# Optimization experiments

Measured on AMD Instinct MI355X. Metric: run time of the kernel, lower is better.

## Reference

```python
import jax, jax.numpy as jnp
import numpy as np

NV, NE = 4096, 8192
FV, FE = 128, 64
FV_OUT = 128


def setup_inputs() -> dict:
    key = jax.random.key(0)
    ks = jax.random.split(key, 8)
    stdv = 1.0 / np.sqrt(FV_OUT)
    return {
        "H_v": jax.random.normal(ks[0], (NV, FV), dtype=jnp.float32),
        "H_e": jax.random.normal(ks[1], (NE, FE), dtype=jnp.float32),
        "adj_e": jax.random.uniform(ks[2], (NE, NE), dtype=jnp.float32),
        "adj_v": jax.random.uniform(ks[3], (NV, NV), dtype=jnp.float32),
        "T": jax.random.uniform(ks[4], (NV, NE), dtype=jnp.float32),
        "weight": jax.random.uniform(ks[5], (FV, FV_OUT), minval=-stdv, maxval=stdv, dtype=jnp.float32),
        "p": jax.random.normal(ks[6], (1, FE), dtype=jnp.float32),
        "bias": jax.random.uniform(ks[7], (FV_OUT,), minval=-stdv, maxval=stdv, dtype=jnp.float32),
    }


def reference(H_v, H_e, adj_e, adj_v, T, weight, p, bias):
    # node_layer=True path of GraphConvolution.forward
    # d = (H_e @ p.T) as a vector over edges; T @ diag(d) == T * d[None, :]
    d = (H_e @ p.T)[:, 0]                       # [Ne]
    multiplier = (T * d[None, :]) @ T.T         # [Nv, Nv]
    n = multiplier.shape[0]
    mask = jnp.eye(n, dtype=multiplier.dtype)   # eye mask: diag -> 1, off-diag -> multiplier
    M1 = mask + (1.0 - mask) * multiplier
    adjusted_A = M1 * adj_v                     # elementwise mask with dense adjacency
    output = adjusted_A @ (H_v @ weight) + bias # [Nv, Fv_out]
    return (output, H_e)
```

## Files before the change

kernel.cpp:

```cpp
#include <hip/hip_runtime.h>
#include <stdint.h>

#define NV 4096
#define NE 8192
#define FV 128
#define FE 64
#define FOUT 128

typedef unsigned short u16;
typedef __attribute__((ext_vector_type(8))) short short8;
typedef __attribute__((ext_vector_type(4))) float f32x4;
typedef __attribute__((ext_vector_type(4))) unsigned short u16x4;

__device__ __forceinline__ u16 f2bf(float f) {
  uint32_t u = __builtin_bit_cast(uint32_t, f);
  u += 0x7fffu + ((u >> 16) & 1u);
  return (u16)(u >> 16);
}
__device__ __forceinline__ float bf2f(u16 h) {
  return __builtin_bit_cast(float, (uint32_t)h << 16);
}

#define AS1(p) ((__attribute__((address_space(1))) void*)(void*)(p))
#define AS3(p) ((__attribute__((address_space(3))) void*)(p))

__global__ __launch_bounds__(256) void k_edge_dot(const float* __restrict__ He,
                                                  const float* __restrict__ p,
                                                  float* __restrict__ d,
                                                  float* __restrict__ out) {
  const int lane = threadIdx.x & 63;
  const int gw = blockIdx.x * 4 + (threadIdx.x >> 6);
  const float pv = p[lane];
  for (int e = gw; e < NE; e += 512) {
    float h = He[(size_t)e * FE + lane];
    out[(size_t)NV * FOUT + (size_t)e * FE + lane] = h;
    float v = h * pv;
    #pragma unroll
    for (int off = 32; off > 0; off >>= 1) v += __shfl_down(v, off);
    if (lane == 0) d[e] = v;
  }
}

__global__ __launch_bounds__(256) void k_convert(const float* __restrict__ T,
                                                 const float* __restrict__ d,
                                                 u16* __restrict__ Ta,
                                                 u16* __restrict__ Tb) {
  size_t idx = ((size_t)blockIdx.x * 256 + threadIdx.x) * 8;
  f32x4 t0 = *(const f32x4*)&T[idx];
  f32x4 t1 = *(const f32x4*)&T[idx + 4];
  int e = (int)(idx & (NE - 1));
  f32x4 d0 = *(const f32x4*)&d[e];
  f32x4 d1 = *(const f32x4*)&d[e + 4];
  short8 a, b;
  a[0] = (short)f2bf(t0.x * d0.x); a[1] = (short)f2bf(t0.y * d0.y);
  a[2] = (short)f2bf(t0.z * d0.z); a[3] = (short)f2bf(t0.w * d0.w);
  a[4] = (short)f2bf(t1.x * d1.x); a[5] = (short)f2bf(t1.y * d1.y);
  a[6] = (short)f2bf(t1.z * d1.z); a[7] = (short)f2bf(t1.w * d1.w);
  b[0] = (short)f2bf(t0.x); b[1] = (short)f2bf(t0.y);
  b[2] = (short)f2bf(t0.z); b[3] = (short)f2bf(t0.w);
  b[4] = (short)f2bf(t1.x); b[5] = (short)f2bf(t1.y);
  b[6] = (short)f2bf(t1.z); b[7] = (short)f2bf(t1.w);
  *(short8*)&Ta[idx] = a;
  *(short8*)&Tb[idx] = b;
}

__global__ __launch_bounds__(256) void k_hw(const float* __restrict__ Hv,
                                            const float* __restrict__ W,
                                            u16* __restrict__ HWt) {
  __shared__ float sW[FV * FOUT];
  __shared__ float sH[8 * FV];
  const int tid = threadIdx.x;
  const int i0 = blockIdx.x * 8;
  #pragma unroll
  for (int k = 0; k < 16; ++k)
    *(f32x4*)&sW[k * 1024 + tid * 4] = *(const f32x4*)&W[k * 1024 + tid * 4];
  *(f32x4*)&sH[tid * 4] = *(const f32x4*)&Hv[(size_t)i0 * FV + tid * 4];
  __syncthreads();
  const int n = tid & 127;
  const int rh = tid >> 7;
  float acc[4] = {0.f, 0.f, 0.f, 0.f};
  #pragma unroll 4
  for (int f = 0; f < FV; ++f) {
    float wv = sW[f * FOUT + n];
    #pragma unroll
    for (int rr = 0; rr < 4; ++rr)
      acc[rr] += sH[(rh * 4 + rr) * FV + f] * wv;
  }
  #pragma unroll
  for (int rr = 0; rr < 4; ++rr)
    HWt[(size_t)n * NV + i0 + rh * 4 + rr] = f2bf(acc[rr]);
}

__global__ __launch_bounds__(512, 2) void k_gemm_m(const u16* __restrict__ Ta,
                                                   const u16* __restrict__ Tb,
                                                   const float* __restrict__ adjv,
                                                   u16* __restrict__ adjA) {
  __shared__ __align__(16) u16 smem[66560];

  const int bi = blockIdx.x >> 4;
  const int bj = blockIdx.x & 15;
  const int tile_m = bi * 256;
  const int tile_n = bj * 256;
  const int tid = threadIdx.x;
  const int lane = tid & 63;
  const int wid = tid >> 6;
  const int wr = wid >> 2;
  const int wc = wid & 3;
  const int row16 = lane & 15;
  const int quad = lane >> 4;
  const int swz8 = (quad ^ ((row16 >> 1) & 3)) * 8;

  const int srow = tid >> 2;
  const int sslot = (tid & 3) ^ ((tid >> 3) & 3);
  const u16* gA0 = Ta + (size_t)(tile_m + srow) * NE + sslot * 8;
  const u16* gA1 = gA0 + (size_t)128 * NE;
  const u16* gB0 = Tb + (size_t)(tile_n + srow) * NE + sslot * 8;
  const u16* gB1 = gB0 + (size_t)128 * NE;
  const int ldsO0 = (wid * 64) * 8;
  const int ldsO1 = (512 + wid * 64) * 8;

#define STG(gp0, gp1, roff, kcol)                                                                 \
  do {                                                                                            \
    __builtin_amdgcn_global_load_lds(AS1((gp0) + (kcol)), AS3(&smem[(roff) + ldsO0]), 16, 0, 0);  \
    __builtin_amdgcn_global_load_lds(AS1((gp1) + (kcol)), AS3(&smem[(roff) + ldsO1]), 16, 0, 0);  \
  } while (0)

  f32x4 acc[8][4] = {};
  short8 aX[4], aY[4], bX[4], bY[4];

  const int arow32 = (wr * 128 + row16) * 32 + swz8;
  const int brow32 = (wc * 64 + row16) * 32 + swz8;

#define LDSA(b, kk, mh, DST)                                                                   \
  do { _Pragma("unroll")                                                                       \
    for (int m2 = 0; m2 < 4; ++m2)                                                             \
      DST[m2] = *(const short8*)&smem[(b)*16384 + (kk)*8192 + arow32 + ((mh)*4 + m2) * 512];   \
  } while (0)

#define LDSB(b, kk, DST)                                                                       \
  do { _Pragma("unroll")                                                                       \
    for (int ni = 0; ni < 4; ++ni)                                                             \
      DST[ni] = *(const short8*)&smem[32768 + (b)*16384 + (kk)*8192 + brow32 + ni * 512];      \
  } while (0)

#define MMP(mh, ASET, BSET)                                                                                 \
  do { _Pragma("unroll")                                                                                    \
    for (int m2 = 0; m2 < 4; ++m2) { _Pragma("unroll")                                                      \
      for (int ni = 0; ni < 4; ++ni)                                                                        \
        acc[(mh)*4+m2][ni] = __builtin_amdgcn_mfma_f32_16x16x32_bf16(ASET[m2], BSET[ni], acc[(mh)*4+m2][ni], 0,0,0); \
    }                                                                                                       \
  } while (0)

#define BARF()  do { __builtin_amdgcn_s_barrier(); asm volatile("" ::: "memory"); } while (0)
#define WAITK(k) do { asm volatile("s_waitcnt lgkmcnt(" #k ")" ::: "memory"); \
                      __builtin_amdgcn_sched_barrier(0); } while (0)
#define GATE8() asm volatile("s_waitcnt vmcnt(8)" ::: "memory")
#define PRIO1() __builtin_amdgcn_s_setprio(1)
#define PRIO0() __builtin_amdgcn_s_setprio(0)

  STG(gB0, gB1, 32768, 0);
  STG(gA0, gA1, 0,     0);
  STG(gB0, gB1, 40960, 32);
  STG(gA0, gA1, 8192,  32);
  STG(gB0, gB1, 49152, 64);
  STG(gA0, gA1, 16384, 64);
  STG(gB0, gB1, 57344, 96);
  asm volatile("s_waitcnt vmcnt(10)" ::: "memory");
  BARF();
  LDSB(0, 0, bX);
  LDSA(0, 0, 0, aX);

  #pragma unroll 1
  for (int it = 0; it < 64; ++it) {
    const int t = it * 2;
    const int k1 = (t + 1) * 64;
    const int k2 = (t + 2 < 128 ? t + 2 : 127) * 64;
    const int k3 = (t + 3 < 128 ? t + 3 : 127) * 64;

    LDSA(0, 0, 1, aY);
    STG(gA0, gA1, 24576, k1 + 32);
    WAITK(4);
    PRIO1(); MMP(0, aX, bX); PRIO0();
    GATE8(); BARF();

    LDSB(0, 1, bY); LDSA(0, 1, 0, aX);
    STG(gB0, gB1, 32768, k2);
    WAITK(8);
    PRIO1(); MMP(1, aY, bX); PRIO0();
    BARF();

    LDSA(0, 1, 1, aY);
    STG(gA0, gA1, 0, k2);
    WAITK(4);
    PRIO1(); MMP(0, aX, bY); PRIO0();
    GATE8(); BARF();

    LDSB(1, 0, bX); LDSA(1, 0, 0, aX);
    STG(gB0, gB1, 40960, k2 + 32);
    WAITK(8);
    PRIO1(); MMP(1, aY, bY); PRIO0();
    BARF();

    LDSA(1, 0, 1, aY);
    STG(gA0, gA1, 8192, k2 + 32);
    WAITK(4);
    PRIO1(); MMP(0, aX, bX); PRIO0();
    GATE8(); BARF();

    LDSB(1, 1, bY); LDSA(1, 1, 0, aX);
    STG(gB0, gB1, 49152, k3);
    WAITK(8);
    PRIO1(); MMP(1, aY, bX); PRIO0();
    BARF();

    LDSA(1, 1, 1, aY);
    STG(gA0, gA1, 16384, k3);
    WAITK(4);
    PRIO1(); MMP(0, aX, bY); PRIO0();
    GATE8(); BARF();

    LDSB(0, 0, bX); LDSA(0, 0, 0, aX);
    STG(gB0, gB1, 57344, k3 + 32);
    WAITK(8);
    PRIO1(); MMP(1, aY, bY); PRIO0();
    BARF();
  }

  asm volatile("s_waitcnt vmcnt(0) lgkmcnt(0)" ::: "memory");
  __syncthreads();
  #pragma unroll
  for (int mi = 0; mi < 8; ++mi) {
    #pragma unroll
    for (int ni = 0; ni < 4; ++ni) {
      const int row = wr * 128 + mi * 16 + quad * 4;
      const int col = wc * 64 + ni * 16 + row16;
      #pragma unroll
      for (int r = 0; r < 4; ++r)
        smem[(row + r) * 260 + col] = f2bf(acc[mi][ni][r]);
    }
  }
  __syncthreads();
  const int ep_r = tid >> 4;
  const int ep_c = (tid & 15) * 4;
  for (int pass = 0; pass < 8; ++pass) {
    const int row = pass * 32 + ep_r;
    const int gr = tile_m + row;
    const size_t gbase = (size_t)gr * NV + tile_n;
    #pragma unroll
    for (int j = 0; j < 4; ++j) {
      const int col = ep_c + j * 64;
      const int gc = tile_n + col;
      u16x4 m4 = *(const u16x4*)&smem[row * 260 + col];
      f32x4 av = *(const f32x4*)&adjv[gbase + col];
      u16x4 o;
      o.x = f2bf(((gr == gc + 0) ? 1.0f : bf2f(m4.x)) * av.x);
      o.y = f2bf(((gr == gc + 1) ? 1.0f : bf2f(m4.y)) * av.y);
      o.z = f2bf(((gr == gc + 2) ? 1.0f : bf2f(m4.z)) * av.z);
      o.w = f2bf(((gr == gc + 3) ? 1.0f : bf2f(m4.w)) * av.w);
      *(u16x4*)&adjA[gbase + col] = o;
    }
  }

#undef STG
#undef LDSA
#undef LDSB
#undef MMP
#undef BARF
#undef WAITK
#undef GATE8
#undef PRIO1
#undef PRIO0
}

#define KSPLIT 8
__global__ __launch_bounds__(256) void k_gemm_out(const u16* __restrict__ A,
                                                  const u16* __restrict__ B,
                                                  float* __restrict__ part) {
  __shared__ __align__(16) u16 lA[128 * 32];
  __shared__ __align__(16) u16 lB[128 * 32];
  const int K = NV;
  const int tile_m = blockIdx.y * 128;
  const int kbeg = blockIdx.x * (K / KSPLIT);
  const int kend = kbeg + (K / KSPLIT);
  const int tid = threadIdx.x;
  const int lane = tid & 63;
  const int wave = tid >> 6;
  const int wm = (wave >> 1) * 64;
  const int wn = (wave & 1) * 64;
  const int row16 = lane & 15;
  const int quad = lane >> 4;

  f32x4 acc[4][4] = {};

  for (int k0 = kbeg; k0 < kend; k0 += 32) {
    __syncthreads();
    #pragma unroll
    for (int r = 0; r < 2; ++r) {
      const int chunk = r * 256 + wave * 64 + lane;
      const int row = chunk >> 2;
      const int cc = chunk & 3;
      const u16* ga = A + ((size_t)(tile_m + row) * K + k0 + cc * 8);
      const u16* gb = B + ((size_t)row * K + k0 + cc * 8);
      __builtin_amdgcn_global_load_lds(AS1(ga), AS3(&lA[(r * 256 + wave * 64) * 8]), 16, 0, 0);
      __builtin_amdgcn_global_load_lds(AS1(gb), AS3(&lB[(r * 256 + wave * 64) * 8]), 16, 0, 0);
    }
    __syncthreads();
    short8 a[4], b[4];
    #pragma unroll
    for (int mi = 0; mi < 4; ++mi)
      a[mi] = *(const short8*)&lA[(wm + mi * 16 + row16) * 32 + quad * 8];
    #pragma unroll
    for (int ni = 0; ni < 4; ++ni)
      b[ni] = *(const short8*)&lB[(wn + ni * 16 + row16) * 32 + quad * 8];
    #pragma unroll
    for (int mi = 0; mi < 4; ++mi)
      #pragma unroll
      for (int ni = 0; ni < 4; ++ni)
        acc[mi][ni] = __builtin_amdgcn_mfma_f32_16x16x32_bf16(a[mi], b[ni], acc[mi][ni], 0, 0, 0);
  }

  float* pdst = part + (size_t)blockIdx.x * NV * FOUT;
  #pragma unroll
  for (int mi = 0; mi < 4; ++mi) {
    #pragma unroll
    for (int ni = 0; ni < 4; ++ni) {
      const int gc = wn + ni * 16 + row16;
      #pragma unroll
      for (int r = 0; r < 4; ++r) {
        const int gr = tile_m + wm + mi * 16 + quad * 4 + r;
        pdst[(size_t)gr * FOUT + gc] = acc[mi][ni][r];
      }
    }
  }
}

__global__ __launch_bounds__(256) void k_reduce(const float* __restrict__ part,
                                                const float* __restrict__ bias,
                                                float* __restrict__ out) {
  size_t idx = ((size_t)blockIdx.x * 256 + threadIdx.x) * 4;
  f32x4 s = *(const f32x4*)&bias[idx & (FOUT - 1)];
  #pragma unroll
  for (int ks = 0; ks < KSPLIT; ++ks)
    s += *(const f32x4*)&part[(size_t)ks * NV * FOUT + idx];
  *(f32x4*)&out[idx] = s;
}

extern "C" void kernel_launch(void* const* d_in, const int* in_sizes, int n_in,
                              void* d_out, int out_size, void* d_ws, size_t ws_size,
                              hipStream_t stream) {
  const float* Hv   = (const float*)d_in[0];
  const float* He   = (const float*)d_in[1];
  const float* adjv = (const float*)d_in[3];
  const float* T    = (const float*)d_in[4];
  const float* W    = (const float*)d_in[5];
  const float* p    = (const float*)d_in[6];
  const float* bias = (const float*)d_in[7];
  float* out = (float*)d_out;

  char* ws = (char*)d_ws;
  float* dvec = (float*)ws;
  u16* HWt    = (u16*)(ws + ((size_t)1 << 20));
  u16* Ta     = (u16*)(ws + ((size_t)2 << 20));
  u16* Tb     = (u16*)(ws + ((size_t)2 << 20) + ((size_t)64 << 20));
  u16* adjA   = (u16*)(ws + ((size_t)2 << 20) + ((size_t)128 << 20));
  float* part = (float*)(ws + ((size_t)2 << 20) + ((size_t)160 << 20));

  k_edge_dot<<<128, 256, 0, stream>>>(He, p, dvec, out);
  k_convert<<<(NV * NE) / (256 * 8), 256, 0, stream>>>(T, dvec, Ta, Tb);
  k_hw<<<NV / 8, 256, 0, stream>>>(Hv, W, HWt);
  k_gemm_m<<<256, 512, 0, stream>>>(Ta, Tb, adjv, adjA);
  k_gemm_out<<<dim3(KSPLIT, NV / 128), 256, 0, stream>>>(adjA, HWt, part);
  k_reduce<<<(NV * FOUT) / (256 * 4), 256, 0, stream>>>(part, bias, out);
}
```

Measured before the change: 674.7 us.

## Switch multiplier GEMM to 32x32x16 MFMA with restructured LDS swizzle and waits

Replaces the 16x16x32 bf16 MFMA tiling in the T·diag(d)·T^T GEMM with 32x32x16 MFMA instructions. This changes the per-wave fragment layout, the LDS read swizzle, the staging slot swizzle and the epilogue register-to-row mapping. It also drops register double-buffering of fragments in favour of load-then-wait (lgkmcnt(0)) with an extra barrier per phase, and removes the unroll-1 pragma. The larger MFMA shape cuts LDS reads per FLOP and instruction count. In exchange, the full lgkm waits and extra barriers serialize LDS loads against MFMA work.

```diff
diff --git a/kernel.cpp b/kernel.cpp
--- a/kernel.cpp
+++ b/kernel.cpp
@@ -10,6 +10,7 @@
 typedef unsigned short u16;
 typedef __attribute__((ext_vector_type(8))) short short8;
 typedef __attribute__((ext_vector_type(4))) float f32x4;
+typedef __attribute__((ext_vector_type(16))) float f32x16;
 typedef __attribute__((ext_vector_type(4))) unsigned short u16x4;
 
 __device__ __forceinline__ u16 f2bf(float f) {
@@ -106,12 +107,14 @@
   const int wid = tid >> 6;
   const int wr = wid >> 2;
   const int wc = wid & 3;
-  const int row16 = lane & 15;
-  const int quad = lane >> 4;
-  const int swz8 = (quad ^ ((row16 >> 1) & 3)) * 8;
+  const int row32 = lane & 31;
+  const int hi = lane >> 5;
+
+  const int swz0 = ((hi)     ^ (row32 & 3)) * 8;
+  const int swz1 = ((2 + hi) ^ (row32 & 3)) * 8;
 
   const int srow = tid >> 2;
-  const int sslot = (tid & 3) ^ ((tid >> 3) & 3);
+  const int sslot = (tid & 3) ^ ((tid >> 2) & 3);
   const u16* gA0 = Ta + (size_t)(tile_m + srow) * NE + sslot * 8;
   const u16* gA1 = gA0 + (size_t)128 * NE;
   const u16* gB0 = Tb + (size_t)(tile_n + srow) * NE + sslot * 8;
@@ -125,36 +128,45 @@
     __builtin_amdgcn_global_load_lds(AS1((gp1) + (kcol)), AS3(&smem[(roff) + ldsO1]), 16, 0, 0);  \
   } while (0)
 
-  f32x4 acc[8][4] = {};
-  short8 aX[4], aY[4], bX[4], bY[4];
-
-  const int arow32 = (wr * 128 + row16) * 32 + swz8;
-  const int brow32 = (wc * 64 + row16) * 32 + swz8;
-
-#define LDSA(b, kk, mh, DST)                                                                   \
-  do { _Pragma("unroll")                                                                       \
-    for (int m2 = 0; m2 < 4; ++m2)                                                             \
-      DST[m2] = *(const short8*)&smem[(b)*16384 + (kk)*8192 + arow32 + ((mh)*4 + m2) * 512];   \
+  f32x16 acc[4][2] = {};
+  short8 aF[2][2], bF[2][2];
+
+  const int arow32 = (wr * 128 + row32) * 32;
+  const int brow32 = (wc * 64 + row32) * 32;
+
+#define LDSA(b, kk, mh)                                                                            \
+  do { _Pragma("unroll")                                                                           \
+    for (int m2 = 0; m2 < 2; ++m2) {                                                               \
+      const int ab = (b)*16384 + (kk)*8192 + arow32 + ((mh)*2 + m2) * 1024;                        \
+      aF[m2][0] = *(const short8*)&smem[ab + swz0];                                                \
+      aF[m2][1] = *(const short8*)&smem[ab + swz1];                                                \
+    }                                                                                              \
   } while (0)
 
-#define LDSB(b, kk, DST)                                                                       \
-  do { _Pragma("unroll")                                                                       \
-    for (int ni = 0; ni < 4; ++ni)                                                             \
-      DST[ni] = *(const short8*)&smem[32768 + (b)*16384 + (kk)*8192 + brow32 + ni * 512];      \
+#define LDSB(b, kk)                                                                                \
+  do { _Pragma("unroll")                                                                           \
+    for (int ni = 0; ni < 2; ++ni) {                                                               \
+      const int bb = 32768 + (b)*16384 + (kk)*8192 + brow32 + ni * 1024;                           \
+      bF[ni][0] = *(const short8*)&smem[bb + swz0];                                                \
+      bF[ni][1] = *(const short8*)&smem[bb + swz1];                                                \
+    }                                                                                              \
   } while (0)
 
-#define MMP(mh, ASET, BSET)                                                                                 \
-  do { _Pragma("unroll")                                                                                    \
-    for (int m2 = 0; m2 < 4; ++m2) { _Pragma("unroll")                                                      \
-      for (int ni = 0; ni < 4; ++ni)                                                                        \
-        acc[(mh)*4+m2][ni] = __builtin_amdgcn_mfma_f32_16x16x32_bf16(ASET[m2], BSET[ni], acc[(mh)*4+m2][ni], 0,0,0); \
-    }                                                                                                       \
+#define MMH(mh)                                                                                    \
+  do { _Pragma("unroll")                                                                           \
+    for (int k16 = 0; k16 < 2; ++k16) { _Pragma("unroll")                                          \
+      for (int m2 = 0; m2 < 2; ++m2) { _Pragma("unroll")                                           \
+        for (int ni = 0; ni < 2; ++ni)                                                             \
+          acc[(mh)*2+m2][ni] = __builtin_amdgcn_mfma_f32_32x32x16_bf16(                            \
+              aF[m2][k16], bF[ni][k16], acc[(mh)*2+m2][ni], 0, 0, 0);                              \
+      }                                                                                            \
+    }                                                                                              \
   } while (0)
 
 #define BARF()  do { __builtin_amdgcn_s_barrier(); asm volatile("" ::: "memory"); } while (0)
-#define WAITK(k) do { asm volatile("s_waitcnt lgkmcnt(" #k ")" ::: "memory"); \
-                      __builtin_amdgcn_sched_barrier(0); } while (0)
-#define GATE8() asm volatile("s_waitcnt vmcnt(8)" ::: "memory")
+#define LGKM0() do { asm volatile("s_waitcnt lgkmcnt(0)" ::: "memory"); \
+                     __builtin_amdgcn_sched_barrier(0); } while (0)
+#define VM6()   asm volatile("s_waitcnt vmcnt(6)" ::: "memory")
 #define PRIO1() __builtin_amdgcn_s_setprio(1)
 #define PRIO0() __builtin_amdgcn_s_setprio(0)
 
@@ -165,78 +177,79 @@
   STG(gB0, gB1, 49152, 64);
   STG(gA0, gA1, 16384, 64);
   STG(gB0, gB1, 57344, 96);
-  asm volatile("s_waitcnt vmcnt(10)" ::: "memory");
+  VM6();
   BARF();
-  LDSB(0, 0, bX);
-  LDSA(0, 0, 0, aX);
-
-  #pragma unroll 1
+
   for (int it = 0; it < 64; ++it) {
     const int t = it * 2;
     const int k1 = (t + 1) * 64;
     const int k2 = (t + 2 < 128 ? t + 2 : 127) * 64;
     const int k3 = (t + 3 < 128 ? t + 3 : 127) * 64;
 
-    LDSA(0, 0, 1, aY);
+    LDSB(0, 0); LDSA(0, 0, 0);
     STG(gA0, gA1, 24576, k1 + 32);
-    WAITK(4);
-    PRIO1(); MMP(0, aX, bX); PRIO0();
-    GATE8(); BARF();
-
-    LDSB(0, 1, bY); LDSA(0, 1, 0, aX);
+    BAR_P1: BARF(); LGKM0();
+    PRIO1(); MMH(0); PRIO0();
+    BARF();
+
+    LDSA(0, 0, 1);
     STG(gB0, gB1, 32768, k2);
-    WAITK(8);
-    PRIO1(); MMP(1, aY, bX); PRIO0();
-    BARF();
-
-    LDSA(0, 1, 1, aY);
+    BARF(); LGKM0();
+    PRIO1(); MMH(1); PRIO0();
+    BARF();
+
+    LDSB(0, 1); LDSA(0, 1, 0);
     STG(gA0, gA1, 0, k2);
-    WAITK(4);
-    PRIO1(); MMP(0, aX, bY); PRIO0();
-    GATE8(); BARF();
-
-    LDSB(1, 0, bX); LDSA(1, 0, 0, aX);
+    BARF(); LGKM0();
+    PRIO1(); MMH(0); PRIO0();
+    BARF();
+
+    LDSA(0, 1, 1);
     STG(gB0, gB1, 40960, k2 + 32);
-    WAITK(8);
-    PRIO1(); MMP(1, aY, bY); PRIO0();
-    BARF();
-
-    LDSA(1, 0, 1, aY);
+    BARF(); LGKM0();
+    PRIO1(); MMH(1); PRIO0();
+    VM6();
+    BARF();
+
+    LDSB(1, 0); LDSA(1, 0, 0);
     STG(gA0, gA1, 8192, k2 + 32);
-    WAITK(4);
-    PRIO1(); MMP(0, aX, bX); PRIO0();
-    GATE8(); BARF();
-
-    LDSB(1, 1, bY); LDSA(1, 1, 0, aX);
+    BARF(); LGKM0();
+    PRIO1(); MMH(0); PRIO0();
+    BARF();
+
+    LDSA(1, 0, 1);
     STG(gB0, gB1, 49152, k3);
-    WAITK(8);
-    PRIO1(); MMP(1, aY, bX); PRIO0();
-    BARF();
-
-    LDSA(1, 1, 1, aY);
+    BARF(); LGKM0();
+    PRIO1(); MMH(1); PRIO0();
+    BARF();
+
+    LDSB(1, 1); LDSA(1, 1, 0);
     STG(gA0, gA1, 16384, k3);
-    WAITK(4);
-    PRIO1(); MMP(0, aX, bY); PRIO0();
-    GATE8(); BARF();
-
-    LDSB(0, 0, bX); LDSA(0, 0, 0, aX);
+    BARF(); LGKM0();
+    PRIO1(); MMH(0); PRIO0();
+    BARF();
+
+    LDSA(1, 1, 1);
     STG(gB0, gB1, 57344, k3 + 32);
-    WAITK(8);
-    PRIO1(); MMP(1, aY, bY); PRIO0();
+    BARF(); LGKM0();
+    PRIO1(); MMH(1); PRIO0();
+    VM6();
     BARF();
   }
 
   asm volatile("s_waitcnt vmcnt(0) lgkmcnt(0)" ::: "memory");
   __syncthreads();
   #pragma unroll
-  for (int mi = 0; mi < 8; ++mi) {
-    #pragma unroll
-    for (int ni = 0; ni < 4; ++ni) {
-      const int row = wr * 128 + mi * 16 + quad * 4;
-      const int col = wc * 64 + ni * 16 + row16;
+  for (int mi = 0; mi < 4; ++mi) {
+    #pragma unroll
+    for (int ni = 0; ni < 2; ++ni) {
+      const int colb = wc * 64 + ni * 32 + row32;
+      const int rowb = wr * 128 + mi * 32 + 4 * hi;
       #pragma unroll
-      for (int r = 0; r < 4; ++r)
-        smem[(row + r) * 260 + col] = f2bf(acc[mi][ni][r]);
+      for (int reg = 0; reg < 16; ++reg) {
+        const int row = rowb + (reg & 3) + 8 * (reg >> 2);
+        smem[row * 260 + colb] = f2bf(acc[mi][ni][reg]);
+      }
     }
   }
   __syncthreads();
@@ -264,10 +277,10 @@
 #undef STG
 #undef LDSA
 #undef LDSB
-#undef MMP
+#undef MMH
 #undef BARF
-#undef WAITK
-#undef GATE8
+#undef LGKM0
+#undef VM6
 #undef PRIO1
 #undef PRIO0
 }
```

Result: slower. 735.7 us (+9.0%).
